# Kernel optimization log

Hardware: AMD Instinct MI355X
Metric: run time of the kernel (lower is better)

The kernel has to match this reference:

```python
import jax, jax.numpy as jnp
import numpy as np

DIM1, DIM2, NUM_ANS = 1024, 1024, 1000
B, T = 64, 128


def setup_inputs() -> dict:
    key = jax.random.key(0)
    ks = jax.random.split(key, 12)
    H, D_IN = DIM1, DIM1 + DIM2
    s = 0.02
    return {
        "data1": jax.random.normal(ks[0], (B, T, DIM1), dtype=jnp.float32),
        "data2": jax.random.normal(ks[1], (B, T, DIM2), dtype=jnp.float32),
        # layer-1 LSTM (input D_IN -> hidden H), PyTorch gate order i,f,g,o
        "W_ih1": jax.random.normal(ks[2], (4 * H, D_IN), dtype=jnp.float32) * s,
        "W_hh1": jax.random.normal(ks[3], (4 * H, H), dtype=jnp.float32) * s,
        "b1": jax.random.normal(ks[4], (4 * H,), dtype=jnp.float32) * s,
        # layer-2 LSTM (H -> H)
        "W_ih2": jax.random.normal(ks[5], (4 * H, H), dtype=jnp.float32) * s,
        "W_hh2": jax.random.normal(ks[6], (4 * H, H), dtype=jnp.float32) * s,
        "b2": jax.random.normal(ks[7], (4 * H,), dtype=jnp.float32) * s,
        # predict MLP: dim1 -> dim1//4 -> num_ans
        "Wp1": jax.random.normal(ks[8], (DIM1, DIM1 // 4), dtype=jnp.float32) * s,
        "bp1": jnp.zeros((DIM1 // 4,), dtype=jnp.float32),
        "Wp2": jax.random.normal(ks[9], (DIM1 // 4, NUM_ANS), dtype=jnp.float32) * s,
        "bp2": jnp.zeros((NUM_ANS,), dtype=jnp.float32),
    }


def _lstm_cell(x, h, c, Wih, Whh, b):
    gates = x @ Wih.T + h @ Whh.T + b  # [B, 4H]
    i, f, g, o = jnp.split(gates, 4, axis=-1)
    c_new = jax.nn.sigmoid(f) * c + jax.nn.sigmoid(i) * jnp.tanh(g)
    h_new = jax.nn.sigmoid(o) * jnp.tanh(c_new)
    return h_new, c_new


def reference(data1, data2, W_ih1, W_hh1, b1, W_ih2, W_hh2, b2, Wp1, bp1, Wp2, bp2):
    joint = jnp.concatenate((data1, data2), axis=-1)  # [B, T, dim1+dim2]
    Bb = joint.shape[0]
    H = W_hh1.shape[1]
    z = jnp.zeros((Bb, H), dtype=joint.dtype)

    def step(carry, x_t):
        h1, c1, h2, c2 = carry
        h1, c1 = _lstm_cell(x_t, h1, c1, W_ih1, W_hh1, b1)
        h2, c2 = _lstm_cell(h1, h2, c2, W_ih2, W_hh2, b2)
        out_t = h2 + h1  # residual connection between layers
        return (h1, c1, h2, c2), out_t

    xs = jnp.swapaxes(joint, 0, 1)  # [T, B, D]
    _, outs = jax.lax.scan(step, (z, z, z, z), xs)
    lstm_out = jnp.swapaxes(outs, 0, 1)  # [B, T, H]

    hid = jax.nn.relu(lstm_out @ Wp1 + bp1)  # dropout is identity at inference
    logits = hid @ Wp2 + bp2  # [B, T, num_ans]
    return jax.nn.softmax(jnp.squeeze(logits), axis=-1)
```

## Files before the change

kernel.cpp:

```cpp
#include <hip/hip_runtime.h>
#include <math.h>

#define BB   64
#define TT   128
#define HH   1024
#define DIN  2048
#define G4   4096
#define MALL 8192
#define NANS 1000

typedef __attribute__((ext_vector_type(8))) short bf16x8;
typedef __attribute__((ext_vector_type(4))) float f32x4;

__device__ __forceinline__ float sigmoidf_(float x) { return 1.0f / (1.0f + expf(-x)); }

__device__ __forceinline__ unsigned short f2bf(float f) {
  unsigned u = __float_as_uint(f);
  u = (u + 0x7fff + ((u >> 16) & 1)) >> 16;
  return (unsigned short)u;
}
__device__ __forceinline__ float bf2f(unsigned short h) {
  return __uint_as_float(((unsigned)h) << 16);
}
__device__ __forceinline__ f32x4 mfma16(bf16x8 a, bf16x8 b, f32x4 c) {
  return __builtin_amdgcn_mfma_f32_16x16x32_bf16(a, b, c, 0, 0, 0);
}

__global__ __launch_bounds__(256) void concat_cast(
    const float* __restrict__ a, const float* __restrict__ b,
    unsigned short* __restrict__ o, int rshift, long total)
{
  long idx = ((long)blockIdx.x * 256 + threadIdx.x) * 4;
  if (idx >= total) return;
  int row = (int)(idx >> rshift);
  int col = (int)(idx & ((1L << rshift) - 1));
  int half = 1 << (rshift - 1);
  const float* s = (col < half) ? (a + (size_t)row * half + col)
                                : (b + (size_t)row * half + col - half);
  float4 v = *(const float4*)s;
  ushort4 ov;
  ov.x = f2bf(v.x); ov.y = f2bf(v.y); ov.z = f2bf(v.z); ov.w = f2bf(v.w);
  *(ushort4*)(o + idx) = ov;
}

__global__ __launch_bounds__(256) void cast_bf16(
    const float* __restrict__ s, unsigned short* __restrict__ o, long n)
{
  long idx = ((long)blockIdx.x * 256 + threadIdx.x) * 4;
  if (idx >= n) return;
  float4 v = *(const float4*)(s + idx);
  ushort4 ov;
  ov.x = f2bf(v.x); ov.y = f2bf(v.y); ov.z = f2bf(v.z); ov.w = f2bf(v.w);
  *(ushort4*)(o + idx) = ov;
}

__global__ __launch_bounds__(256) void cvt_wp1(
    const float* __restrict__ Wp1, unsigned short* __restrict__ o)
{
  int idx = blockIdx.x * 256 + threadIdx.x;
  int n = idx >> 10, k = idx & 1023;
  o[idx] = f2bf(Wp1[(size_t)k * 256 + n]);
}

__global__ __launch_bounds__(256) void cvt_wp2(
    const float* __restrict__ Wp2, unsigned short* __restrict__ o)
{
  int idx = blockIdx.x * 256 + threadIdx.x;
  int n = idx >> 8, k = idx & 255;
  o[idx] = f2bf(n < NANS ? Wp2[(size_t)k * NANS + n] : 0.f);
}

__global__ __launch_bounds__(256) void zero_f4(float4* __restrict__ p)
{
  p[blockIdx.x * 256 + threadIdx.x] = make_float4(0.f, 0.f, 0.f, 0.f);
}

template<int OUT_BF16, int RELU, int PERM>
__global__ __launch_bounds__(256) void mfma_gemm(
    const unsigned short* __restrict__ A,
    const unsigned short* __restrict__ W,
    const float* __restrict__ bias,
    void* __restrict__ Cout,
    int M, int N, int K, int ldc, int nvalid)
{
  __shared__ __align__(16) unsigned short As[128 * 72];
  __shared__ __align__(16) unsigned short Bs[128 * 72];
  const int t = threadIdx.x;
  const int n0 = blockIdx.x * 128, m0 = blockIdx.y * 128;
  const int w = t >> 6, lane = t & 63, lr = lane & 15, q = lane >> 4;
  const int wn = (w & 1) * 64, wm = (w >> 1) * 64;
  f32x4 acc[4][4] = {};
  for (int k0 = 0; k0 < K; k0 += 64) {
    #pragma unroll
    for (int s = 0; s < 4; s++) {
      int ci = s * 256 + t;
      int row = ci >> 3, c = ci & 7;
      bf16x8 va = *(const bf16x8*)(A + (size_t)(m0 + row) * K + k0 + c * 8);
      *(bf16x8*)(As + row * 72 + c * 8) = va;
      bf16x8 vb = *(const bf16x8*)(W + (size_t)(n0 + row) * K + k0 + c * 8);
      *(bf16x8*)(Bs + row * 72 + c * 8) = vb;
    }
    __syncthreads();
    #pragma unroll
    for (int kk = 0; kk < 2; kk++) {
      bf16x8 a[4], b[4];
      #pragma unroll
      for (int mt = 0; mt < 4; mt++)
        a[mt] = *(const bf16x8*)(As + (wm + mt * 16 + lr) * 72 + kk * 32 + q * 8);
      #pragma unroll
      for (int nt = 0; nt < 4; nt++)
        b[nt] = *(const bf16x8*)(Bs + (wn + nt * 16 + lr) * 72 + kk * 32 + q * 8);
      #pragma unroll
      for (int mt = 0; mt < 4; mt++)
        #pragma unroll
        for (int nt = 0; nt < 4; nt++)
          acc[mt][nt] = mfma16(a[mt], b[nt], acc[mt][nt]);
    }
    __syncthreads();
  }
  #pragma unroll
  for (int mt = 0; mt < 4; mt++)
    #pragma unroll
    for (int nt = 0; nt < 4; nt++)
      #pragma unroll
      for (int r = 0; r < 4; r++) {
        int row = m0 + wm + mt * 16 + q * 4 + r;
        int col = n0 + wn + nt * 16 + lr;
        if (col < nvalid) {
          float v = acc[mt][nt][r] + bias[col];
          if (RELU) v = fmaxf(v, 0.f);
          if (PERM) row = ((row & 127) << 6) | (row >> 7);
          if (OUT_BF16)
            ((unsigned short*)Cout)[(size_t)row * ldc + col] = f2bf(v);
          else
            ((float*)Cout)[(size_t)row * ldc + col] = v;
        }
      }
}

__global__ __launch_bounds__(256) void lstm_stepA(
    const unsigned short* __restrict__ hprev,
    const unsigned short* __restrict__ Wb,
    const unsigned short* __restrict__ gxb,
    int tstep,
    unsigned short* hcur,
    float* __restrict__ c1)
{
  __shared__ float red[4][64][17];
  const int t = threadIdx.x;
  const int w = t >> 6, lane = t & 63, lr = lane & 15, q = lane >> 4;
  const int j0 = blockIdx.x * 4;
  {
    const int g = lr >> 2, u0 = lr & 3;
    const unsigned short* wp = Wb + (size_t)(g * 1024 + j0 + u0) * 1024;
    f32x4 acc[4] = {};
    const int kb = w * 256;
    #pragma unroll
    for (int ks = 0; ks < 8; ks++) {
      int k = kb + ks * 32 + q * 8;
      bf16x8 bfrag = *(const bf16x8*)(wp + k);
      #pragma unroll
      for (int mt = 0; mt < 4; mt++) {
        bf16x8 afrag = *(const bf16x8*)(hprev + (size_t)(mt * 16 + lr) * 2048 + k);
        acc[mt] = mfma16(afrag, bfrag, acc[mt]);
      }
    }
    #pragma unroll
    for (int mt = 0; mt < 4; mt++)
      #pragma unroll
      for (int r = 0; r < 4; r++)
        red[w][mt * 16 + q * 4 + r][lr] = acc[mt][r];
  }
  __syncthreads();
  const int m = t >> 2, u = t & 3;
  float s[4];
  #pragma unroll
  for (int g = 0; g < 4; g++)
    s[g] = red[0][m][g * 4 + u] + red[1][m][g * 4 + u]
         + red[2][m][g * 4 + u] + red[3][m][g * 4 + u];
  const unsigned short* gp = gxb + (size_t)((tstep << 6) + m) * 4096 + j0 + u;
  s[0] += bf2f(gp[0]); s[1] += bf2f(gp[1024]);
  s[2] += bf2f(gp[2048]); s[3] += bf2f(gp[3072]);
  const int ju = j0 + u;
  float i_ = sigmoidf_(s[0]), f_ = sigmoidf_(s[1]);
  float g_ = tanhf(s[2]), o_ = sigmoidf_(s[3]);
  float c = f_ * c1[m * 1024 + ju] + i_ * g_;
  c1[m * 1024 + ju] = c;
  hcur[(size_t)m * 2048 + ju] = f2bf(o_ * tanhf(c));
}

__global__ __launch_bounds__(256) void lstm_stepB(
    const unsigned short* __restrict__ hprev,
    unsigned short* hcur,
    const unsigned short* __restrict__ W2,
    const float* __restrict__ b2,
    int tstep,
    float* __restrict__ c2,
    unsigned short* __restrict__ lob)
{
  __shared__ float red[4][64][17];
  const int t = threadIdx.x;
  const int w = t >> 6, lane = t & 63, lr = lane & 15, q = lane >> 4;
  const int j0 = blockIdx.x * 4;
  {
    const int g = lr >> 2, u0 = lr & 3;
    const unsigned short* wp = W2 + (size_t)(g * 1024 + j0 + u0) * 2048;
    f32x4 acc[4] = {};
    const int kb = w * 512;
    #pragma unroll
    for (int ks = 0; ks < 16; ks++) {
      int k = kb + ks * 32 + q * 8;
      bf16x8 bfrag = *(const bf16x8*)(wp + k);
      const unsigned short* hsrc = (k < 1024) ? hcur : hprev;
      #pragma unroll
      for (int mt = 0; mt < 4; mt++) {
        bf16x8 afrag = *(const bf16x8*)(hsrc + (size_t)(mt * 16 + lr) * 2048 + k);
        acc[mt] = mfma16(afrag, bfrag, acc[mt]);
      }
    }
    #pragma unroll
    for (int mt = 0; mt < 4; mt++)
      #pragma unroll
      for (int r = 0; r < 4; r++)
        red[w][mt * 16 + q * 4 + r][lr] = acc[mt][r];
  }
  __syncthreads();
  const int m = t >> 2, u = t & 3;
  const int ju = j0 + u;
  float s[4];
  #pragma unroll
  for (int g = 0; g < 4; g++)
    s[g] = red[0][m][g * 4 + u] + red[1][m][g * 4 + u]
         + red[2][m][g * 4 + u] + red[3][m][g * 4 + u]
         + b2[g * 1024 + ju];
  float i_ = sigmoidf_(s[0]), f_ = sigmoidf_(s[1]);
  float g_ = tanhf(s[2]), o_ = sigmoidf_(s[3]);
  float c = f_ * c2[m * 1024 + ju] + i_ * g_;
  c2[m * 1024 + ju] = c;
  float h2v = o_ * tanhf(c);
  hcur[(size_t)m * 2048 + 1024 + ju] = f2bf(h2v);
  float h1v = bf2f(hcur[(size_t)m * 2048 + ju]);
  lob[(size_t)((m << 7) + tstep) * 1024 + ju] = f2bf(h1v + h2v);
}

__global__ __launch_bounds__(256) void softmax_k(float* __restrict__ out)
{
  __shared__ float smax[4];
  __shared__ float ssum[4];
  const int m = blockIdx.x;
  const int t = threadIdx.x;
  const int lane = t & 63, wid = t >> 6;
  const bool act = (t < 250);
  float x[4] = {0.f, 0.f, 0.f, 0.f};
  if (act) *(float4*)x = *(const float4*)(out + (size_t)m * NANS + t * 4);
  float v = act ? fmaxf(fmaxf(x[0], x[1]), fmaxf(x[2], x[3])) : -1e30f;
  #pragma unroll
  for (int o = 32; o > 0; o >>= 1) v = fmaxf(v, __shfl_down(v, o));
  if (lane == 0) smax[wid] = v;
  __syncthreads();
  const float mx = fmaxf(fmaxf(smax[0], smax[1]), fmaxf(smax[2], smax[3]));
  float e[4] = {0.f, 0.f, 0.f, 0.f};
  float s = 0.f;
  if (act) {
    e[0] = expf(x[0] - mx); e[1] = expf(x[1] - mx);
    e[2] = expf(x[2] - mx); e[3] = expf(x[3] - mx);
    s = (e[0] + e[1]) + (e[2] + e[3]);
  }
  #pragma unroll
  for (int o = 32; o > 0; o >>= 1) s += __shfl_down(s, o);
  if (lane == 0) ssum[wid] = s;
  __syncthreads();
  const float inv = 1.0f / (((ssum[0] + ssum[1]) + (ssum[2] + ssum[3])));
  if (act) {
    float4 o4 = make_float4(e[0] * inv, e[1] * inv, e[2] * inv, e[3] * inv);
    *(float4*)(out + (size_t)m * NANS + t * 4) = o4;
  }
}

extern "C" void kernel_launch(void* const* d_in, const int* in_sizes, int n_in,
                              void* d_out, int out_size, void* d_ws, size_t ws_size,
                              hipStream_t stream)
{
  const float* d1   = (const float*)d_in[0];
  const float* d2   = (const float*)d_in[1];
  const float* Wih1 = (const float*)d_in[2];
  const float* Whh1 = (const float*)d_in[3];
  const float* b1   = (const float*)d_in[4];
  const float* Wih2 = (const float*)d_in[5];
  const float* Whh2 = (const float*)d_in[6];
  const float* b2   = (const float*)d_in[7];
  const float* Wp1  = (const float*)d_in[8];
  const float* bp1  = (const float*)d_in[9];
  const float* Wp2  = (const float*)d_in[10];
  const float* bp2  = (const float*)d_in[11];
  float* out = (float*)d_out;

  unsigned char* p = (unsigned char*)d_ws;
  unsigned short* gxb   = (unsigned short*)p;  p += 67108864;
  unsigned short* jb    = (unsigned short*)p;  p += 33554432;
  unsigned short* Wb1   = (unsigned short*)p;  p += 16777216;
  unsigned short* W2cat = (unsigned short*)p;  p += 16777216;
  unsigned short* Whh1b = (unsigned short*)p;  p += 8388608;
  unsigned short* lob   = (unsigned short*)p;  p += 16777216;
  unsigned short* hidb  = (unsigned short*)p;  p += 4194304;
  unsigned short* Wp1t  = (unsigned short*)p;  p += 524288;
  unsigned short* Wp2t  = (unsigned short*)p;  p += 524288;
  unsigned short* H0    = (unsigned short*)p;  p += 262144;
  float*          c1    = (float*)p;           p += 262144;
  float*          c2    = (float*)p;           p += 262144;
  unsigned short* H1    = (unsigned short*)p;  p += 262144;
  if (ws_size < (size_t)(p - (unsigned char*)d_ws)) return;

  concat_cast<<<16384, 256, 0, stream>>>(d1, d2, jb, 11, 16777216L);
  cast_bf16<<<8192, 256, 0, stream>>>(Wih1, Wb1, 8388608L);
  cast_bf16<<<4096, 256, 0, stream>>>(Whh1, Whh1b, 4194304L);
  concat_cast<<<8192, 256, 0, stream>>>(Wih2, Whh2, W2cat, 11, 8388608L);
  cvt_wp1<<<1024, 256, 0, stream>>>(Wp1, Wp1t);
  cvt_wp2<<<1024, 256, 0, stream>>>(Wp2, Wp2t);
  zero_f4<<<192, 256, 0, stream>>>((float4*)H0);

  mfma_gemm<1, 0, 1><<<dim3(32, 64), 256, 0, stream>>>(
      jb, Wb1, b1, gxb, MALL, G4, DIN, G4, G4);

  for (int t = 0; t < TT; t++) {
    unsigned short* hp = (t & 1) ? H1 : H0;
    unsigned short* hc = (t & 1) ? H0 : H1;
    lstm_stepA<<<256, 256, 0, stream>>>(hp, Whh1b, gxb, t, hc, c1);
    lstm_stepB<<<256, 256, 0, stream>>>(hp, hc, W2cat, b2, t, c2, lob);
  }

  mfma_gemm<1, 1, 0><<<dim3(2, 64), 256, 0, stream>>>(
      lob, Wp1t, bp1, hidb, MALL, 256, 1024, 256, 256);
  mfma_gemm<0, 0, 0><<<dim3(8, 64), 256, 0, stream>>>(
      hidb, Wp2t, bp2, out, MALL, 1024, 256, NANS, NANS);
  softmax_k<<<MALL, 256, 0, stream>>>(out);
}
```

Measured before the change: 3.180 ms.

## Fuse LSTM time loop into persistent cooperative kernel with register-resident weights

Replaces the 256 per-timestep kernel launches with a single cooperative kernel of 512 blocks. Half the blocks run layer 1 and half run layer 2, with layer 2 one step behind so both layers advance in the same phase between grid-wide barriers. Each block loads its recurrent weight slice into registers once, and the cell state stays in registers for the whole loop. This removes per-launch overhead and repeated weight reloads, at the cost of grid.sync latency and a residency requirement of two blocks per CU; the old multi-launch path is kept as a fallback if the cooperative launch fails.

After: 9.666 ms. 3.04x slower.

```diff
diff --git a/kernel.cpp b/kernel.cpp
--- a/kernel.cpp
+++ b/kernel.cpp
@@ -1,4 +1,5 @@
 #include <hip/hip_runtime.h>
+#include <hip/hip_cooperative_groups.h>
 #include <math.h>
 
 #define BB   64
@@ -138,13 +139,112 @@
       }
 }
 
+__global__ __launch_bounds__(256, 2) void lstm_loop(
+    const unsigned short* __restrict__ Whh1b,
+    const unsigned short* __restrict__ W2cat,
+    const unsigned short* __restrict__ gxb,
+    const float* __restrict__ b2,
+    unsigned short* __restrict__ hbuf,
+    unsigned short* __restrict__ lob)
+{
+  cooperative_groups::grid_group grid = cooperative_groups::this_grid();
+  __shared__ float red[4][64][17];
+  const int t = threadIdx.x;
+  const int w = t >> 6, lane = t & 63, lr = lane & 15, q = lane >> 4;
+  const bool isA = (blockIdx.x < 256);
+  const int j0 = (isA ? blockIdx.x : blockIdx.x - 256) * 4;
+  const int g0 = lr >> 2, u0 = lr & 3;
+  const int cm = t >> 2, cu = t & 3, ju = j0 + cu;
+
+  bf16x8 wreg[16];
+  float b2r[4] = {0.f, 0.f, 0.f, 0.f};
+  if (isA) {
+    const unsigned short* wp =
+        Whh1b + (size_t)(g0 * 1024 + j0 + u0) * 1024 + w * 256 + q * 8;
+    #pragma unroll
+    for (int ks = 0; ks < 8; ks++) wreg[ks] = *(const bf16x8*)(wp + ks * 32);
+  } else {
+    const unsigned short* wp =
+        W2cat + (size_t)(g0 * 1024 + j0 + u0) * 2048 + w * 512 + q * 8;
+    #pragma unroll
+    for (int ks = 0; ks < 16; ks++) wreg[ks] = *(const bf16x8*)(wp + ks * 32);
+    #pragma unroll
+    for (int gg = 0; gg < 4; gg++) b2r[gg] = b2[gg * 1024 + ju];
+  }
+  float creg = 0.f;
+
+  for (int p = 0; p <= TT; p++) {
+    const unsigned short* hprev = hbuf + (size_t)((p + 1) & 1) * 131072;
+    unsigned short*       hc    = hbuf + (size_t)(p & 1) * 131072;
+    if (isA) {
+      if (p < TT) {
+        const unsigned short* gp = gxb + ((size_t)(p << 6) + cm) * 4096 + ju;
+        unsigned short gi = gp[0], gf = gp[1024], gg2 = gp[2048], go = gp[3072];
+        f32x4 acc[4] = {};
+        const unsigned short* hb = hprev + w * 256 + q * 8;
+        #pragma unroll
+        for (int ks = 0; ks < 8; ks++)
+          #pragma unroll
+          for (int mt = 0; mt < 4; mt++) {
+            bf16x8 af = *(const bf16x8*)(hb + (size_t)(mt * 16 + lr) * 2048 + ks * 32);
+            acc[mt] = mfma16(af, wreg[ks], acc[mt]);
+          }
+        #pragma unroll
+        for (int mt = 0; mt < 4; mt++)
+          #pragma unroll
+          for (int r = 0; r < 4; r++)
+            red[w][mt * 16 + q * 4 + r][lr] = acc[mt][r];
+        __syncthreads();
+        float s[4];
+        #pragma unroll
+        for (int gg = 0; gg < 4; gg++)
+          s[gg] = red[0][cm][gg * 4 + cu] + red[1][cm][gg * 4 + cu]
+                + red[2][cm][gg * 4 + cu] + red[3][cm][gg * 4 + cu];
+        s[0] += bf2f(gi); s[1] += bf2f(gf); s[2] += bf2f(gg2); s[3] += bf2f(go);
+        float i_ = sigmoidf_(s[0]), f_ = sigmoidf_(s[1]);
+        float g_ = tanhf(s[2]), o_ = sigmoidf_(s[3]);
+        creg = f_ * creg + i_ * g_;
+        hc[(size_t)cm * 2048 + ju] = f2bf(o_ * tanhf(creg));
+      }
+    } else {
+      if (p >= 1) {
+        f32x4 acc[4] = {};
+        const unsigned short* hb = hprev + w * 512 + q * 8;
+        #pragma unroll
+        for (int ks = 0; ks < 16; ks++)
+          #pragma unroll
+          for (int mt = 0; mt < 4; mt++) {
+            bf16x8 af = *(const bf16x8*)(hb + (size_t)(mt * 16 + lr) * 2048 + ks * 32);
+            acc[mt] = mfma16(af, wreg[ks], acc[mt]);
+          }
+        #pragma unroll
+        for (int mt = 0; mt < 4; mt++)
+          #pragma unroll
+          for (int r = 0; r < 4; r++)
+            red[w][mt * 16 + q * 4 + r][lr] = acc[mt][r];
+        __syncthreads();
+        float s[4];
+        #pragma unroll
+        for (int gg = 0; gg < 4; gg++)
+          s[gg] = red[0][cm][gg * 4 + cu] + red[1][cm][gg * 4 + cu]
+                + red[2][cm][gg * 4 + cu] + red[3][cm][gg * 4 + cu] + b2r[gg];
+        float i_ = sigmoidf_(s[0]), f_ = sigmoidf_(s[1]);
+        float g_ = tanhf(s[2]), o_ = sigmoidf_(s[3]);
+        creg = f_ * creg + i_ * g_;
+        float h2v = o_ * tanhf(creg);
+        hc[(size_t)cm * 2048 + 1024 + ju] = f2bf(h2v);
+        float h1v = bf2f(hprev[(size_t)cm * 2048 + ju]);
+        lob[((size_t)(cm << 7) + (p - 1)) * 1024 + ju] = f2bf(h1v + h2v);
+      }
+    }
+    if (p < TT) grid.sync();
+  }
+}
+
 __global__ __launch_bounds__(256) void lstm_stepA(
-    const unsigned short* __restrict__ hprev,
-    const unsigned short* __restrict__ Wb,
-    const unsigned short* __restrict__ gxb,
-    int tstep,
-    unsigned short* hcur,
-    float* __restrict__ c1)
+    const unsigned short* __restrict__ hprev, const unsigned short* __restrict__ Wb,
+    const unsigned short* __restrict__ gxb, int tstep,
+    unsigned short* hcur, float* __restrict__ c1)
 {
   __shared__ float red[4][64][17];
   const int t = threadIdx.x;
@@ -190,13 +290,9 @@
 }
 
 __global__ __launch_bounds__(256) void lstm_stepB(
-    const unsigned short* __restrict__ hprev,
-    unsigned short* hcur,
-    const unsigned short* __restrict__ W2,
-    const float* __restrict__ b2,
-    int tstep,
-    float* __restrict__ c2,
-    unsigned short* __restrict__ lob)
+    const unsigned short* __restrict__ hprev, unsigned short* hcur,
+    const unsigned short* __restrict__ W2, const float* __restrict__ b2,
+    int tstep, float* __restrict__ c2, unsigned short* __restrict__ lob)
 {
   __shared__ float red[4][64][17];
   const int t = threadIdx.x;
@@ -305,10 +401,9 @@
   unsigned short* hidb  = (unsigned short*)p;  p += 4194304;
   unsigned short* Wp1t  = (unsigned short*)p;  p += 524288;
   unsigned short* Wp2t  = (unsigned short*)p;  p += 524288;
-  unsigned short* H0    = (unsigned short*)p;  p += 262144;
+  unsigned short* hbuf  = (unsigned short*)p;  p += 524288;
   float*          c1    = (float*)p;           p += 262144;
   float*          c2    = (float*)p;           p += 262144;
-  unsigned short* H1    = (unsigned short*)p;  p += 262144;
   if (ws_size < (size_t)(p - (unsigned char*)d_ws)) return;
 
   concat_cast<<<16384, 256, 0, stream>>>(d1, d2, jb, 11, 16777216L);
@@ -317,16 +412,26 @@
   concat_cast<<<8192, 256, 0, stream>>>(Wih2, Whh2, W2cat, 11, 8388608L);
   cvt_wp1<<<1024, 256, 0, stream>>>(Wp1, Wp1t);
   cvt_wp2<<<1024, 256, 0, stream>>>(Wp2, Wp2t);
-  zero_f4<<<192, 256, 0, stream>>>((float4*)H0);
+  zero_f4<<<256, 256, 0, stream>>>((float4*)hbuf);
 
   mfma_gemm<1, 0, 1><<<dim3(32, 64), 256, 0, stream>>>(
       jb, Wb1, b1, gxb, MALL, G4, DIN, G4, G4);
 
-  for (int t = 0; t < TT; t++) {
-    unsigned short* hp = (t & 1) ? H1 : H0;
-    unsigned short* hc = (t & 1) ? H0 : H1;
-    lstm_stepA<<<256, 256, 0, stream>>>(hp, Whh1b, gxb, t, hc, c1);
-    lstm_stepB<<<256, 256, 0, stream>>>(hp, hc, W2cat, b2, t, c2, lob);
+  {
+    void* args[] = {(void*)&Whh1b, (void*)&W2cat, (void*)&gxb, (void*)&b2,
+                    (void*)&hbuf, (void*)&lob};
+    hipError_t ce = hipLaunchCooperativeKernel((void*)lstm_loop, dim3(512),
+                                               dim3(256), args, 0, stream);
+    if (ce != hipSuccess) {
+      unsigned short* H0 = hbuf;
+      unsigned short* H1 = hbuf + 131072;
+      for (int t = 0; t < TT; t++) {
+        unsigned short* hp = (t & 1) ? H1 : H0;
+        unsigned short* hc = (t & 1) ? H0 : H1;
+        lstm_stepA<<<256, 256, 0, stream>>>(hp, Whh1b, gxb, t, hc, c1);
+        lstm_stepB<<<256, 256, 0, stream>>>(hp, hc, W2cat, b2, t, c2, lob);
+      }
+    }
   }
 
   mfma_gemm<1, 1, 0><<<dim3(2, 64), 256, 0, stream>>>(
```

## Skew LSTM layers into one launch per phase running layer1 t and layer2 t-1

Applied to the files above, without the earlier changes.

Replaces the two kernel launches per timestep (layer-1 then layer-2) with a single launch per phase. In that launch 256 blocks compute layer 1 for step p while another 256 compute layer 2 for step p-1, using a double-buffered h buffer that holds [h1|h2] per row. This halves the number of serial launches and lets the two layers' weight streaming run concurrently across more CUs. The cost is one extra phase and in-place writes of h2 into the previous buffer, which needs care with buffer aliasing.

Result: faster. 2.803 ms (-11.9%).

```diff
diff --git a/kernel.cpp b/kernel.cpp
--- a/kernel.cpp
+++ b/kernel.cpp
@@ -138,109 +138,100 @@
       }
 }
 
-__global__ __launch_bounds__(256) void lstm_stepA(
-    const unsigned short* __restrict__ hprev,
-    const unsigned short* __restrict__ Wb,
+__global__ __launch_bounds__(256) void lstm_phase(
+    const unsigned short* __restrict__ Whh1b,
+    const unsigned short* __restrict__ W2cat,
     const unsigned short* __restrict__ gxb,
-    int tstep,
-    unsigned short* hcur,
-    float* __restrict__ c1)
+    const float* __restrict__ b2,
+    int p,
+    unsigned short* __restrict__ hbuf,
+    float* __restrict__ c1, float* __restrict__ c2,
+    unsigned short* __restrict__ lob)
 {
   __shared__ float red[4][64][17];
   const int t = threadIdx.x;
   const int w = t >> 6, lane = t & 63, lr = lane & 15, q = lane >> 4;
-  const int j0 = blockIdx.x * 4;
-  {
-    const int g = lr >> 2, u0 = lr & 3;
-    const unsigned short* wp = Wb + (size_t)(g * 1024 + j0 + u0) * 1024;
-    f32x4 acc[4] = {};
-    const int kb = w * 256;
-    #pragma unroll
-    for (int ks = 0; ks < 8; ks++) {
-      int k = kb + ks * 32 + q * 8;
-      bf16x8 bfrag = *(const bf16x8*)(wp + k);
-      #pragma unroll
-      for (int mt = 0; mt < 4; mt++) {
-        bf16x8 afrag = *(const bf16x8*)(hprev + (size_t)(mt * 16 + lr) * 2048 + k);
-        acc[mt] = mfma16(afrag, bfrag, acc[mt]);
+  const bool isA = (blockIdx.x < 256);
+  const int j0 = (isA ? blockIdx.x : blockIdx.x - 256) * 4;
+  const int g0 = lr >> 2, u0 = lr & 3;
+  const int cm = t >> 2, cu = t & 3, ju = j0 + cu;
+  const unsigned short* hprev = hbuf + (size_t)((p + 1) & 1) * 131072;
+  unsigned short*       hc    = hbuf + (size_t)(p & 1) * 131072;
+
+  if (isA) {
+    if (p == TT) return;
+    const unsigned short* gp = gxb + ((size_t)(p << 6) + cm) * 4096 + ju;
+    unsigned short gi = gp[0], gf = gp[1024], gg2 = gp[2048], go = gp[3072];
+    {
+      const unsigned short* wp =
+          Whh1b + (size_t)(g0 * 1024 + j0 + u0) * 1024 + w * 256 + q * 8;
+      const unsigned short* hb = hprev + w * 256 + q * 8;
+      f32x4 acc[4] = {};
+      #pragma unroll
+      for (int ks = 0; ks < 8; ks++) {
+        bf16x8 bfrag = *(const bf16x8*)(wp + ks * 32);
+        #pragma unroll
+        for (int mt = 0; mt < 4; mt++) {
+          bf16x8 af = *(const bf16x8*)(hb + (size_t)(mt * 16 + lr) * 2048 + ks * 32);
+          acc[mt] = mfma16(af, bfrag, acc[mt]);
+        }
       }
+      #pragma unroll
+      for (int mt = 0; mt < 4; mt++)
+        #pragma unroll
+        for (int r = 0; r < 4; r++)
+          red[w][mt * 16 + q * 4 + r][lr] = acc[mt][r];
     }
-    #pragma unroll
-    for (int mt = 0; mt < 4; mt++)
-      #pragma unroll
-      for (int r = 0; r < 4; r++)
-        red[w][mt * 16 + q * 4 + r][lr] = acc[mt][r];
+    __syncthreads();
+    float s[4];
+    #pragma unroll
+    for (int gg = 0; gg < 4; gg++)
+      s[gg] = red[0][cm][gg * 4 + cu] + red[1][cm][gg * 4 + cu]
+            + red[2][cm][gg * 4 + cu] + red[3][cm][gg * 4 + cu];
+    s[0] += bf2f(gi); s[1] += bf2f(gf); s[2] += bf2f(gg2); s[3] += bf2f(go);
+    float i_ = sigmoidf_(s[0]), f_ = sigmoidf_(s[1]);
+    float g_ = tanhf(s[2]), o_ = sigmoidf_(s[3]);
+    float c = f_ * c1[cm * 1024 + ju] + i_ * g_;
+    c1[cm * 1024 + ju] = c;
+    hc[(size_t)cm * 2048 + ju] = f2bf(o_ * tanhf(c));
+  } else {
+    if (p == 0) return;
+    {
+      const unsigned short* wp =
+          W2cat + (size_t)(g0 * 1024 + j0 + u0) * 2048 + w * 512 + q * 8;
+      const unsigned short* hb = hprev + w * 512 + q * 8;
+      f32x4 acc[4] = {};
+      #pragma unroll
+      for (int ks = 0; ks < 16; ks++) {
+        bf16x8 bfrag = *(const bf16x8*)(wp + ks * 32);
+        #pragma unroll
+        for (int mt = 0; mt < 4; mt++) {
+          bf16x8 af = *(const bf16x8*)(hb + (size_t)(mt * 16 + lr) * 2048 + ks * 32);
+          acc[mt] = mfma16(af, bfrag, acc[mt]);
+        }
+      }
+      #pragma unroll
+      for (int mt = 0; mt < 4; mt++)
+        #pragma unroll
+        for (int r = 0; r < 4; r++)
+          red[w][mt * 16 + q * 4 + r][lr] = acc[mt][r];
+    }
+    __syncthreads();
+    float s[4];
+    #pragma unroll
+    for (int gg = 0; gg < 4; gg++)
+      s[gg] = red[0][cm][gg * 4 + cu] + red[1][cm][gg * 4 + cu]
+            + red[2][cm][gg * 4 + cu] + red[3][cm][gg * 4 + cu]
+            + b2[gg * 1024 + ju];
+    float i_ = sigmoidf_(s[0]), f_ = sigmoidf_(s[1]);
+    float g_ = tanhf(s[2]), o_ = sigmoidf_(s[3]);
+    float c = f_ * c2[cm * 1024 + ju] + i_ * g_;
+    c2[cm * 1024 + ju] = c;
+    float h2v = o_ * tanhf(c);
+    ((unsigned short*)hprev)[(size_t)cm * 2048 + 1024 + ju] = f2bf(h2v);
+    float h1v = bf2f(hprev[(size_t)cm * 2048 + ju]);
+    lob[((size_t)(cm << 7) + (p - 1)) * 1024 + ju] = f2bf(h1v + h2v);
   }
-  __syncthreads();
-  const int m = t >> 2, u = t & 3;
-  float s[4];
-  #pragma unroll
-  for (int g = 0; g < 4; g++)
-    s[g] = red[0][m][g * 4 + u] + red[1][m][g * 4 + u]
-         + red[2][m][g * 4 + u] + red[3][m][g * 4 + u];
-  const unsigned short* gp = gxb + (size_t)((tstep << 6) + m) * 4096 + j0 + u;
-  s[0] += bf2f(gp[0]); s[1] += bf2f(gp[1024]);
-  s[2] += bf2f(gp[2048]); s[3] += bf2f(gp[3072]);
-  const int ju = j0 + u;
-  float i_ = sigmoidf_(s[0]), f_ = sigmoidf_(s[1]);
-  float g_ = tanhf(s[2]), o_ = sigmoidf_(s[3]);
-  float c = f_ * c1[m * 1024 + ju] + i_ * g_;
-  c1[m * 1024 + ju] = c;
-  hcur[(size_t)m * 2048 + ju] = f2bf(o_ * tanhf(c));
-}
-
-__global__ __launch_bounds__(256) void lstm_stepB(
-    const unsigned short* __restrict__ hprev,
-    unsigned short* hcur,
-    const unsigned short* __restrict__ W2,
-    const float* __restrict__ b2,
-    int tstep,
-    float* __restrict__ c2,
-    unsigned short* __restrict__ lob)
-{
-  __shared__ float red[4][64][17];
-  const int t = threadIdx.x;
-  const int w = t >> 6, lane = t & 63, lr = lane & 15, q = lane >> 4;
-  const int j0 = blockIdx.x * 4;
-  {
-    const int g = lr >> 2, u0 = lr & 3;
-    const unsigned short* wp = W2 + (size_t)(g * 1024 + j0 + u0) * 2048;
-    f32x4 acc[4] = {};
-    const int kb = w * 512;
-    #pragma unroll
-    for (int ks = 0; ks < 16; ks++) {
-      int k = kb + ks * 32 + q * 8;
-      bf16x8 bfrag = *(const bf16x8*)(wp + k);
-      const unsigned short* hsrc = (k < 1024) ? hcur : hprev;
-      #pragma unroll
-      for (int mt = 0; mt < 4; mt++) {
-        bf16x8 afrag = *(const bf16x8*)(hsrc + (size_t)(mt * 16 + lr) * 2048 + k);
-        acc[mt] = mfma16(afrag, bfrag, acc[mt]);
-      }
-    }
-    #pragma unroll
-    for (int mt = 0; mt < 4; mt++)
-      #pragma unroll
-      for (int r = 0; r < 4; r++)
-        red[w][mt * 16 + q * 4 + r][lr] = acc[mt][r];
-  }
-  __syncthreads();
-  const int m = t >> 2, u = t & 3;
-  const int ju = j0 + u;
-  float s[4];
-  #pragma unroll
-  for (int g = 0; g < 4; g++)
-    s[g] = red[0][m][g * 4 + u] + red[1][m][g * 4 + u]
-         + red[2][m][g * 4 + u] + red[3][m][g * 4 + u]
-         + b2[g * 1024 + ju];
-  float i_ = sigmoidf_(s[0]), f_ = sigmoidf_(s[1]);
-  float g_ = tanhf(s[2]), o_ = sigmoidf_(s[3]);
-  float c = f_ * c2[m * 1024 + ju] + i_ * g_;
-  c2[m * 1024 + ju] = c;
-  float h2v = o_ * tanhf(c);
-  hcur[(size_t)m * 2048 + 1024 + ju] = f2bf(h2v);
-  float h1v = bf2f(hcur[(size_t)m * 2048 + ju]);
-  lob[(size_t)((m << 7) + tstep) * 1024 + ju] = f2bf(h1v + h2v);
 }
 
 __global__ __launch_bounds__(256) void softmax_k(float* __restrict__ out)
@@ -305,10 +296,9 @@
   unsigned short* hidb  = (unsigned short*)p;  p += 4194304;
   unsigned short* Wp1t  = (unsigned short*)p;  p += 524288;
   unsigned short* Wp2t  = (unsigned short*)p;  p += 524288;
-  unsigned short* H0    = (unsigned short*)p;  p += 262144;
+  unsigned short* hbuf  = (unsigned short*)p;  p += 524288;
   float*          c1    = (float*)p;           p += 262144;
   float*          c2    = (float*)p;           p += 262144;
-  unsigned short* H1    = (unsigned short*)p;  p += 262144;
   if (ws_size < (size_t)(p - (unsigned char*)d_ws)) return;
 
   concat_cast<<<16384, 256, 0, stream>>>(d1, d2, jb, 11, 16777216L);
@@ -317,17 +307,14 @@
   concat_cast<<<8192, 256, 0, stream>>>(Wih2, Whh2, W2cat, 11, 8388608L);
   cvt_wp1<<<1024, 256, 0, stream>>>(Wp1, Wp1t);
   cvt_wp2<<<1024, 256, 0, stream>>>(Wp2, Wp2t);
-  zero_f4<<<192, 256, 0, stream>>>((float4*)H0);
+  zero_f4<<<256, 256, 0, stream>>>((float4*)hbuf);
 
   mfma_gemm<1, 0, 1><<<dim3(32, 64), 256, 0, stream>>>(
       jb, Wb1, b1, gxb, MALL, G4, DIN, G4, G4);
 
-  for (int t = 0; t < TT; t++) {
-    unsigned short* hp = (t & 1) ? H1 : H0;
-    unsigned short* hc = (t & 1) ? H0 : H1;
-    lstm_stepA<<<256, 256, 0, stream>>>(hp, Whh1b, gxb, t, hc, c1);
-    lstm_stepB<<<256, 256, 0, stream>>>(hp, hc, W2cat, b2, t, c2, lob);
-  }
+  for (int ph = 0; ph <= TT; ph++)
+    lstm_phase<<<512, 256, 0, stream>>>(Whh1b, W2cat, gxb, b2, ph,
+                                        hbuf, c1, c2, lob);
 
   mfma_gemm<1, 1, 0><<<dim3(2, 64), 256, 0, stream>>>(
       lob, Wp1t, bp1, hidb, MALL, 256, 1024, 256, 256);
```
